# Kernel tuning notes

Hardware: AMD Instinct MI355X
Metric: run time of the kernel (lower is better)

The kernel has to match this reference:

```python
import jax, jax.numpy as jnp
import numpy as np

FX, FY = 7, 7            # AdaptiveMaxPool2d output (c.Global_feature_x/y)
IMG = 1024.0             # original image side; ratio = feat_side / IMG


def setup_inputs() -> dict:
    key = jax.random.key(0)
    k1, k2, k3, k4 = jax.random.split(key, 4)
    feature = jax.random.normal(k1, (1, 512, 64, 64), jnp.float32)
    # boxes in image coords, (x1, y1, x2, y2), guaranteed non-degenerate
    u = jax.random.uniform(k2, (3, 4))
    person_bboxs = jnp.stack([u[:, 0] * 0.4 * IMG, u[:, 1] * 0.4 * IMG,
                              (0.5 + u[:, 2] * 0.4) * IMG, (0.5 + u[:, 3] * 0.4) * IMG], axis=1)
    v = jax.random.uniform(k3, (4, 4))
    obj_bboxs = jnp.stack([v[:, 0] * 0.4 * IMG, v[:, 1] * 0.4 * IMG,
                           (0.5 + v[:, 2] * 0.4) * IMG, (0.5 + v[:, 3] * 0.4) * IMG], axis=1)
    ratio = jnp.array([64.0 / IMG, 64.0 / IMG], jnp.float32)
    D_in = 512 * FX * FY * 6  # 150528
    W_fc = jax.random.normal(k4, (D_in, 1024), jnp.float32) * 0.01
    b_fc = jnp.zeros((1024,), jnp.float32)
    return {"feature": feature, "person_bboxs": person_bboxs, "obj_bboxs": obj_bboxs,
            "ratio": ratio, "W_fc": W_fc, "b_fc": b_fc}


def _adaptive_max_pool(feat, y0, y1, x0, x1):
    """AdaptiveMaxPool2d((FX,FY)) on feat[:, y0:y1, x0:x1], feat: [C,H,W].
    PyTorch bins: start=floor(i*h/FX), end=ceil((i+1)*h/FX). Mask-based so it
    is jit-safe with traced (data-dependent) bounds."""
    Cc, Hh, Ww = feat.shape
    h = y1 - y0
    w = x1 - x0
    i = jnp.arange(FX)
    j = jnp.arange(FY)
    rs = y0 + (i * h) // FX
    re = y0 - ((-(i + 1) * h) // FX)   # ceil div
    cs = x0 + (j * w) // FY
    ce = x0 - ((-(j + 1) * w) // FY)
    ys = jnp.arange(Hh)
    xs = jnp.arange(Ww)
    rmask = (ys[None, :] >= rs[:, None]) & (ys[None, :] < re[:, None])  # [FX,H]
    cmask = (xs[None, :] >= cs[:, None]) & (xs[None, :] < ce[:, None])  # [FY,W]
    neg = jnp.array(-jnp.inf, feat.dtype)
    tmp = jnp.max(jnp.where(rmask[:, None, :, None], feat[None], neg), axis=2)      # [FX,C,W]
    pooled = jnp.max(jnp.where(cmask[None, None, :, :], tmp[:, :, None, :], neg), axis=3)  # [FX,C,FY]
    # torch .view(-1) on [1,C,FX,FY] flattens channel-major
    return jnp.transpose(pooled, (1, 0, 2)).reshape(-1)  # [C*FX*FY]


def reference(feature, person_bboxs, obj_bboxs, ratio, W_fc, b_fc):
    feat = feature[0]  # [C,H,W]
    Cc, Hh, Ww = feat.shape
    scale = jnp.stack([ratio[0], ratio[1], ratio[0], ratio[1]])
    pb = jax.lax.stop_gradient(jnp.round(person_bboxs * scale)).astype(jnp.int32)  # [3,4] x1,y1,x2,y2
    ob = jax.lax.stop_gradient(jnp.round(obj_bboxs * scale)).astype(jnp.int32)     # [4,4]
    scene = _adaptive_max_pool(feat, 0, Hh, 0, Ww)
    human = [_adaptive_max_pool(feat, pb[i, 1], pb[i, 3], pb[i, 0], pb[i, 2]) for i in range(3)]
    objs = []
    for i in range(3):
        for j in range(4):
            objs.append(_adaptive_max_pool(
                feat,
                jnp.minimum(pb[i, 1], ob[j, 1]), jnp.maximum(pb[i, 3], ob[j, 3]),
                jnp.minimum(pb[i, 0], ob[j, 0]), jnp.maximum(pb[i, 2], ob[j, 2])))
    total = jnp.stack([
        jnp.concatenate([human[i], objs[4 * i], objs[4 * i + 1],
                         objs[4 * i + 2], objs[4 * i + 3], scene])
        for i in range(3)])  # [3, 512*FX*FY*6]
    return total @ W_fc + b_fc  # [3, 1024]
```

## Files before the change

### kernel.cpp

```cpp
#include <hip/hip_runtime.h>
#include <math.h>

#define CCH   512
#define HW    64
#define FXY   7
#define BINS  49
#define POOL_LEN (CCH * BINS)
#define NPOOLS 16
#define D_IN  (POOL_LEN * 6)
#define NOUT  1024
#define KPB   147
#define NKB   1024

__device__ __forceinline__ void region_of(int p, const float* pb, const float* ob,
                                          float r0, float r1,
                                          int& x0, int& y0, int& x1, int& y1) {
    if (p == 0) { x0 = 0; y0 = 0; x1 = HW; y1 = HW; return; }
    if (p <= 3) {
        int i = p - 1;
        x0 = (int)rintf(pb[i * 4 + 0] * r0);
        y0 = (int)rintf(pb[i * 4 + 1] * r1);
        x1 = (int)rintf(pb[i * 4 + 2] * r0);
        y1 = (int)rintf(pb[i * 4 + 3] * r1);
        return;
    }
    int i = (p - 4) >> 2, j = (p - 4) & 3;
    int px0 = (int)rintf(pb[i * 4 + 0] * r0), py0 = (int)rintf(pb[i * 4 + 1] * r1);
    int px1 = (int)rintf(pb[i * 4 + 2] * r0), py1 = (int)rintf(pb[i * 4 + 3] * r1);
    int ox0 = (int)rintf(ob[j * 4 + 0] * r0), oy0 = (int)rintf(ob[j * 4 + 1] * r1);
    int ox1 = (int)rintf(ob[j * 4 + 2] * r0), oy1 = (int)rintf(ob[j * 4 + 3] * r1);
    x0 = min(px0, ox0); y0 = min(py0, oy0);
    x1 = max(px1, ox1); y1 = max(py1, oy1);
}

__global__ void init_out(const float* __restrict__ b, float* __restrict__ out) {
    int o = blockIdx.x * blockDim.x + threadIdx.x;
    if (o < 3 * NOUT) out[o] = b[o & (NOUT - 1)];
}

__global__ __launch_bounds__(256) void pool_kernel(
        const float* __restrict__ feat, const float* __restrict__ pb,
        const float* __restrict__ ob, const float* __restrict__ ratio,
        float* __restrict__ pools) {
    int p    = blockIdx.x;
    int wv   = threadIdx.x >> 6;
    int lane = threadIdx.x & 63;
    int c    = blockIdx.y * 4 + wv;

    int x0, y0, x1, y1;
    region_of(p, pb, ob, ratio[0], ratio[1], x0, y0, x1, y1);
    int h = y1 - y0, w = x1 - x0;

    __shared__ float cm[4][FXY][HW];

    const float* f = feat + (size_t)c * (HW * HW);
    #pragma unroll
    for (int i = 0; i < FXY; ++i) {
        int rs = y0 + (i * h) / FXY;
        int re = y0 + ((i + 1) * h + FXY - 1) / FXY;
        float m = -INFINITY;
        if (lane < w) {
            const float* fp = f + rs * HW + x0 + lane;
            for (int y = rs; y < re; ++y, fp += HW) m = fmaxf(m, *fp);
        }
        cm[wv][i][lane] = m;
    }
    __syncthreads();

    if (lane < BINS) {
        int i = lane / FXY, j = lane % FXY;
        int cs = (j * w) / FXY;
        int ce = ((j + 1) * w + FXY - 1) / FXY;
        float m = -INFINITY;
        for (int x = cs; x < ce; ++x) m = fmaxf(m, cm[wv][i][x]);
        pools[(size_t)p * POOL_LEN + c * BINS + lane] = m;
    }
}

__global__ __launch_bounds__(256) void gemv_kernel(
        const float* __restrict__ pools, const float* __restrict__ W,
        float* __restrict__ out) {
    int k0 = blockIdx.x * KPB;
    __shared__ float t[3][KPB];
    for (int kk = threadIdx.x; kk < KPB; kk += 256) {
        int k = k0 + kk;
        int s = k / POOL_LEN, rr = k - s * POOL_LEN;
        #pragma unroll
        for (int m = 0; m < 3; ++m) {
            int pi = (s == 0) ? (1 + m) : ((s == 5) ? 0 : (4 + m * 4 + (s - 1)));
            t[m][kk] = pools[(size_t)pi * POOL_LEN + rr];
        }
    }
    __syncthreads();

    int n0 = threadIdx.x * 4;
    float acc[3][4] = {};
    const float4* Wp = (const float4*)(W + (size_t)k0 * NOUT + n0);
    #pragma unroll 7
    for (int kk = 0; kk < KPB; ++kk) {
        float4 w4 = Wp[(size_t)kk * (NOUT / 4)];
        float t0 = t[0][kk], t1 = t[1][kk], t2 = t[2][kk];
        acc[0][0] += t0 * w4.x; acc[0][1] += t0 * w4.y;
        acc[0][2] += t0 * w4.z; acc[0][3] += t0 * w4.w;
        acc[1][0] += t1 * w4.x; acc[1][1] += t1 * w4.y;
        acc[1][2] += t1 * w4.z; acc[1][3] += t1 * w4.w;
        acc[2][0] += t2 * w4.x; acc[2][1] += t2 * w4.y;
        acc[2][2] += t2 * w4.z; acc[2][3] += t2 * w4.w;
    }
    #pragma unroll
    for (int m = 0; m < 3; ++m) {
        atomicAdd(&out[m * NOUT + n0 + 0], acc[m][0]);
        atomicAdd(&out[m * NOUT + n0 + 1], acc[m][1]);
        atomicAdd(&out[m * NOUT + n0 + 2], acc[m][2]);
        atomicAdd(&out[m * NOUT + n0 + 3], acc[m][3]);
    }
}

extern "C" void kernel_launch(void* const* d_in, const int* in_sizes, int n_in,
                              void* d_out, int out_size, void* d_ws, size_t ws_size,
                              hipStream_t stream) {
    const float* feature = (const float*)d_in[0];
    const float* pb      = (const float*)d_in[1];
    const float* ob      = (const float*)d_in[2];
    const float* ratio   = (const float*)d_in[3];
    const float* W       = (const float*)d_in[4];
    const float* bias    = (const float*)d_in[5];
    float* out   = (float*)d_out;
    float* pools = (float*)d_ws;

    hipLaunchKernelGGL(init_out, dim3(12), dim3(256), 0, stream, bias, out);
    hipLaunchKernelGGL(pool_kernel, dim3(NPOOLS, CCH / 4), dim3(256), 0, stream,
                       feature, pb, ob, ratio, pools);
    hipLaunchKernelGGL(gemv_kernel, dim3(NKB), dim3(256), 0, stream,
                       pools, W, out);
}
```

Baseline: 857.9 us.

## Replace atomic split-K accumulation with partial buffers and a reduction kernel

The GEMV split-K changes from 1024 blocks of 147 rows to 256 blocks of 588 rows. Each block now writes its partial sums to a workspace buffer instead of issuing atomic adds. A new reduce kernel sums the 256 partials per output and adds the bias, which replaces the init kernel. This removes atomic contention and makes the result deterministic, but adds a kernel launch and partial-buffer traffic, and with only 256 blocks the GPU may be underfilled.

```diff
diff --git a/kernel.cpp b/kernel.cpp
--- a/kernel.cpp
+++ b/kernel.cpp
@@ -9,8 +9,8 @@
 #define NPOOLS 16
 #define D_IN  (POOL_LEN * 6)
 #define NOUT  1024
-#define KPB   147
-#define NKB   1024
+#define KPB   588
+#define NKB   256
 
 __device__ __forceinline__ void region_of(int p, const float* pb, const float* ob,
                                           float r0, float r1,
@@ -31,11 +31,6 @@
     int ox1 = (int)rintf(ob[j * 4 + 2] * r0), oy1 = (int)rintf(ob[j * 4 + 3] * r1);
     x0 = min(px0, ox0); y0 = min(py0, oy0);
     x1 = max(px1, ox1); y1 = max(py1, oy1);
-}
-
-__global__ void init_out(const float* __restrict__ b, float* __restrict__ out) {
-    int o = blockIdx.x * blockDim.x + threadIdx.x;
-    if (o < 3 * NOUT) out[o] = b[o & (NOUT - 1)];
 }
 
 __global__ __launch_bounds__(256) void pool_kernel(
@@ -79,8 +74,9 @@
 
 __global__ __launch_bounds__(256) void gemv_kernel(
         const float* __restrict__ pools, const float* __restrict__ W,
-        float* __restrict__ out) {
-    int k0 = blockIdx.x * KPB;
+        float* __restrict__ pf) {
+    int b  = blockIdx.x;
+    int k0 = b * KPB;
     __shared__ float t[3][KPB];
     for (int kk = threadIdx.x; kk < KPB; kk += 256) {
         int k = k0 + kk;
@@ -96,7 +92,7 @@
     int n0 = threadIdx.x * 4;
     float acc[3][4] = {};
     const float4* Wp = (const float4*)(W + (size_t)k0 * NOUT + n0);
-    #pragma unroll 7
+    #pragma unroll 8
     for (int kk = 0; kk < KPB; ++kk) {
         float4 w4 = Wp[(size_t)kk * (NOUT / 4)];
         float t0 = t[0][kk], t1 = t[1][kk], t2 = t[2][kk];
@@ -109,10 +105,34 @@
     }
     #pragma unroll
     for (int m = 0; m < 3; ++m) {
-        atomicAdd(&out[m * NOUT + n0 + 0], acc[m][0]);
-        atomicAdd(&out[m * NOUT + n0 + 1], acc[m][1]);
-        atomicAdd(&out[m * NOUT + n0 + 2], acc[m][2]);
-        atomicAdd(&out[m * NOUT + n0 + 3], acc[m][3]);
+        ((float4*)(pf + (size_t)b * (3 * NOUT) + m * NOUT))[threadIdx.x] =
+            make_float4(acc[m][0], acc[m][1], acc[m][2], acc[m][3]);
+    }
+}
+
+__global__ __launch_bounds__(256) void reduce_kernel(
+        const float* __restrict__ pf, const float* __restrict__ bias,
+        float* __restrict__ out) {
+    int o0 = blockIdx.x * 64;
+    int lo = threadIdx.x & 63;
+    int g  = threadIdx.x >> 6;
+    const float* p = pf + (size_t)(g * 64) * (3 * NOUT) + o0 + lo;
+    float s0 = 0, s1 = 0, s2 = 0, s3 = 0;
+    #pragma unroll 4
+    for (int i = 0; i < 64; i += 4) {
+        s0 += p[(size_t)(i + 0) * (3 * NOUT)];
+        s1 += p[(size_t)(i + 1) * (3 * NOUT)];
+        s2 += p[(size_t)(i + 2) * (3 * NOUT)];
+        s3 += p[(size_t)(i + 3) * (3 * NOUT)];
+    }
+    float s = (s0 + s1) + (s2 + s3);
+    __shared__ float sm[4][64];
+    sm[g][lo] = s;
+    __syncthreads();
+    if (g == 0) {
+        int o = o0 + lo;
+        float tot = (sm[0][lo] + sm[1][lo]) + (sm[2][lo] + sm[3][lo]);
+        out[o] = bias[o & (NOUT - 1)] + tot;
     }
 }
 
@@ -127,10 +147,12 @@
     const float* bias    = (const float*)d_in[5];
     float* out   = (float*)d_out;
     float* pools = (float*)d_ws;
+    float* pf    = pools + (size_t)NPOOLS * POOL_LEN;
 
-    hipLaunchKernelGGL(init_out, dim3(12), dim3(256), 0, stream, bias, out);
     hipLaunchKernelGGL(pool_kernel, dim3(NPOOLS, CCH / 4), dim3(256), 0, stream,
                        feature, pb, ob, ratio, pools);
     hipLaunchKernelGGL(gemv_kernel, dim3(NKB), dim3(256), 0, stream,
-                       pools, W, out);
+                       pools, W, pf);
+    hipLaunchKernelGGL(reduce_kernel, dim3(3 * NOUT / 64), dim3(256), 0, stream,
+                       pf, bias, out);
 }
```

Measured after the change: 820.5 us. 4.4% less time.
